# Performance work log

Measured on AMD Instinct MI355X. Metric: run time of the kernel, lower is better.

Reference implementation:

```python
import jax, jax.numpy as jnp
import numpy as np


def setup_inputs() -> dict:
    key = jax.random.key(0)
    k1, k2, k3 = jax.random.split(key, 3)
    B, H, HKV, S, D = 2, 32, 8, 2048, 128
    q = jax.random.normal(k1, (B, H, S, D), dtype=jnp.float32)
    k = jax.random.normal(k2, (B, HKV, S, D), dtype=jnp.float32)
    v = jax.random.normal(k3, (B, HKV, S, D), dtype=jnp.float32)
    return {"q": q, "k": k, "v": v}


def reference(q, k, v):
    # GQA: query head j attends with KV head j // num_groups (repeat_interleave
    # semantics). Instead of materializing repeated K/V, reshape Q into
    # [B, Hkv, G, S, D] and contract against shared KV heads directly.
    B, H, S, D = q.shape
    Hkv = k.shape[1]
    G = H // Hkv
    qg = q.reshape(B, Hkv, G, S, D)
    scale = 1.0 / jnp.sqrt(jnp.asarray(D, q.dtype))
    # scores: [B, Hkv, G, Sq, Sk]
    scores = jnp.einsum('bhgqd,bhkd->bhgqk', qg, k) * scale
    # is_causal=True: lower-triangular mask
    causal = jnp.tril(jnp.ones((S, S), dtype=bool))
    scores = jnp.where(causal, scores, jnp.finfo(scores.dtype).min)
    attn = jax.nn.softmax(scores, axis=-1)
    out = jnp.einsum('bhgqk,bhkd->bhgqd', attn, v)
    return out.reshape(B, H, S, D)
```

## Files before the change

### kernel.cpp

```cpp
#include <hip/hip_runtime.h>
#include <hip/hip_bf16.h>
#include <cstdint>

typedef __bf16 bf16;
typedef __bf16 bf16x8 __attribute__((ext_vector_type(8)));
typedef float f32x4 __attribute__((ext_vector_type(4)));
typedef __attribute__((address_space(3))) uint32_t lds_u32;
typedef const __attribute__((address_space(1))) uint32_t glb_u32;

#define B_ 2
#define H_ 32
#define HKV_ 8
#define S_ 2048
#define D_ 128
#define QT 128
#define KT 64
#define NQT (S_ / QT)
#define NTILES (S_ / KT)
#define TILE_ELEMS (KT * D_)
#define PST 72
#define NEG_BIG (-1.0e30f)
#define SCL 0.12751745f
#define DEFER_THR 8.0f

__device__ __forceinline__ bf16x8 cvt8p(float4 a, float4 b) {
  bf16x8 r = {(bf16)a.x, (bf16)a.y, (bf16)a.z, (bf16)a.w,
              (bf16)b.x, (bf16)b.y, (bf16)b.z, (bf16)b.w};
  return r;
}
__device__ __forceinline__ bf16x8 cvt8(const float* f) {
  return cvt8p(*(const float4*)f, *(const float4*)(f + 4));
}

__global__ __launch_bounds__(512) void prep(const float* __restrict__ k,
                                            const float* __restrict__ v,
                                            bf16* __restrict__ kws,
                                            bf16* __restrict__ vws) {
  __shared__ float Vf[KT * 129];
  const int blk = blockIdx.x;
  const int bhkv = blk >> 5, tile = blk & 31;
  const float* ks = k + ((size_t)bhkv * S_ + (size_t)tile * KT) * D_;
  const float* vs = v + ((size_t)bhkv * S_ + (size_t)tile * KT) * D_;
  bf16* kd = kws + (size_t)blk * TILE_ELEMS;
  bf16* vd = vws + (size_t)blk * TILE_ELEMS;
  const int t = threadIdx.x;
#pragma unroll
  for (int i = 0; i < 4; ++i) {
    int c = t + 512 * i, row = c >> 5, c4 = c & 31;
    *(float4*)&Vf[row * 129 + c4 * 4] = *(const float4*)(vs + row * D_ + c4 * 4);
  }
#pragma unroll
  for (int i = 0; i < 2; ++i) {
    int chunk = t + 512 * i, row = chunk >> 4, c16 = chunk & 15;
    int e = (c16 ^ (row & 7)) << 3;
    *(bf16x8*)&kd[chunk * 8] = cvt8(ks + row * D_ + e);
  }
  __syncthreads();
#pragma unroll
  for (int i = 0; i < 2; ++i) {
    int chunk = t + 512 * i, d = chunk >> 3, c8 = chunk & 7;
    int k0 = (c8 ^ (d & 7)) << 3;
    bf16x8 val;
#pragma unroll
    for (int kk = 0; kk < 8; ++kk) val[kk] = (bf16)Vf[(k0 + kk) * 129 + d];
    *(bf16x8*)&vd[chunk * 8] = val;
  }
}

__global__ __launch_bounds__(512, 4) void fa_mfma(
    const float* __restrict__ q, const bf16* __restrict__ kws,
    const bf16* __restrict__ vws, float* __restrict__ out) {
  __shared__ bf16 Kb2[2][TILE_ELEMS];
  __shared__ bf16 Vb[TILE_ELEMS];
  __shared__ bf16 Ps[8 * 16 * PST];

  const int tid = threadIdx.x, wave = tid >> 6, lane = tid & 63;
  const int col = lane & 15, quad = lane >> 4;
  const int bid = blockIdx.x;
  const int tqt = (NQT - 1) - (bid >> 6);
  const int bh = bid & 63, b = bh >> 5, h = bh & 31, hkv = h >> 2;
  const int bhkv = b * HKV_ + hkv;

  const float* qh = q + (size_t)(b * H_ + h) * S_ * D_;
  float* oh = out + (size_t)(b * H_ + h) * S_ * D_;
  const bf16* kg = kws + (size_t)(bhkv * NTILES) * TILE_ELEMS;
  const bf16* vg = vws + (size_t)(bhkv * NTILES) * TILE_ELEMS;
  const int q0 = tqt * QT;
  const int jmax = 2 * tqt + 1;

  bf16x8 qf[4];
  {
    const float* qrow = qh + (size_t)(q0 + wave * 16 + col) * D_ + quad * 8;
#pragma unroll
    for (int ks = 0; ks < 4; ++ks) qf[ks] = cvt8(qrow + ks * 32);
  }

  f32x4 o[8];
#pragma unroll
  for (int i = 0; i < 8; ++i) o[i] = (f32x4){0.f, 0.f, 0.f, 0.f};
  float m_i[4], lp[4];
#pragma unroll
  for (int r = 0; r < 4; ++r) { m_i[r] = NEG_BIG; lp[r] = 0.f; }

  const int qoff = (quad * 16) ^ ((col & 7) << 4);
  const int qx[4] = {qoff, qoff ^ 64, qoff ^ 128, qoff ^ 192};

  const int stoff = tid * 16;

  auto stageK = [&](int j, int buf) {
    const char* src = (const char*)(kg + (size_t)j * TILE_ELEMS) + stoff;
    char* dst = (char*)Kb2[buf] + stoff;
#pragma unroll
    for (int i = 0; i < 2; ++i)
      __builtin_amdgcn_global_load_lds((glb_u32*)(src + i * 8192),
                                       (lds_u32*)(dst + i * 8192), 16, 0, 0);
  };
  auto stageV = [&](int j) {
    const char* src = (const char*)(vg + (size_t)j * TILE_ELEMS) + stoff;
    char* dst = (char*)Vb + stoff;
#pragma unroll
    for (int i = 0; i < 2; ++i)
      __builtin_amdgcn_global_load_lds((glb_u32*)(src + i * 8192),
                                       (lds_u32*)(dst + i * 8192), 16, 0, 0);
  };

  stageK(0, 0);
  asm volatile("s_waitcnt vmcnt(0)" ::: "memory");
  __builtin_amdgcn_s_barrier();
  __builtin_amdgcn_sched_barrier(0);

  for (int j = 0; j <= jmax; ++j) {
    const int cur = j & 1;
    stageV(j);
    if (j < jmax) stageK(j + 1, cur ^ 1);

    const char* Kb = (const char*)Kb2[cur];

    float s[4][4];
    __builtin_amdgcn_s_setprio(1);
#pragma unroll
    for (int nt = 0; nt < 4; ++nt) {
      const char* An = Kb + (nt * 16 + col) * 256;
      f32x4 acc = (f32x4){0.f, 0.f, 0.f, 0.f};
#pragma unroll
      for (int ks = 0; ks < 4; ++ks) {
        bf16x8 kf = *(const bf16x8*)(An + qx[ks]);
        acc = __builtin_amdgcn_mfma_f32_16x16x32_bf16(qf[ks], kf, acc, 0, 0, 0);
      }
#pragma unroll
      for (int r = 0; r < 4; ++r) s[nt][r] = acc[r] * SCL;
    }
    __builtin_amdgcn_s_setprio(0);

    if (j >= 2 * tqt) {
      const int rel = j * KT - q0 - wave * 16;
#pragma unroll
      for (int nt = 0; nt < 4; ++nt) {
        int kc = rel + nt * 16 + col;
#pragma unroll
        for (int r = 0; r < 4; ++r)
          if (kc > quad * 4 + r) s[nt][r] = NEG_BIG;
      }
    }

    float mx[4];
#pragma unroll
    for (int r = 0; r < 4; ++r) {
      float m0 = fmaxf(fmaxf(s[0][r], s[1][r]), fmaxf(s[2][r], s[3][r]));
#pragma unroll
      for (int off = 1; off < 16; off <<= 1)
        m0 = fmaxf(m0, __shfl_xor(m0, off, 64));
      mx[r] = m0;
    }
    float need = fmaxf(fmaxf(mx[0] - m_i[0], mx[1] - m_i[1]),
                       fmaxf(mx[2] - m_i[2], mx[3] - m_i[3]));
    if (__any(need > DEFER_THR)) {
#pragma unroll
      for (int r = 0; r < 4; ++r) {
        float mnew = fmaxf(m_i[r], mx[r]);
        float alpha = exp2f(m_i[r] - mnew);
        lp[r] *= alpha;
        m_i[r] = mnew;
#pragma unroll
        for (int dt = 0; dt < 8; ++dt) o[dt][r] *= alpha;
      }
    }

    float p[4][4];
#pragma unroll
    for (int r = 0; r < 4; ++r) {
      float rs = 0.f;
#pragma unroll
      for (int nt = 0; nt < 4; ++nt) {
        float pv = exp2f(s[nt][r] - m_i[r]);
        p[nt][r] = pv;
        rs += pv;
      }
      lp[r] += rs;
    }

    bf16* pw = &Ps[wave * 16 * PST];
#pragma unroll
    for (int nt = 0; nt < 4; ++nt)
#pragma unroll
      for (int r = 0; r < 4; ++r)
        pw[(quad * 4 + r) * PST + nt * 16 + col] = (bf16)p[nt][r];

    if (j < jmax)
      asm volatile("s_waitcnt vmcnt(2) lgkmcnt(0)" ::: "memory");
    else
      asm volatile("s_waitcnt vmcnt(0) lgkmcnt(0)" ::: "memory");
    __builtin_amdgcn_s_barrier();
    __builtin_amdgcn_sched_barrier(0);

    bf16x8 pf[2];
#pragma unroll
    for (int ks = 0; ks < 2; ++ks)
      pf[ks] = *(const bf16x8*)&pw[col * PST + ks * 32 + quad * 8];

    __builtin_amdgcn_s_setprio(1);
#pragma unroll
    for (int dt = 0; dt < 8; ++dt) {
      const char* Av = (const char*)Vb + (dt * 16 + col) * 128;
#pragma unroll
      for (int ks = 0; ks < 2; ++ks) {
        bf16x8 vf = *(const bf16x8*)(Av + qx[ks]);
        o[dt] = __builtin_amdgcn_mfma_f32_16x16x32_bf16(pf[ks], vf, o[dt], 0, 0, 0);
      }
    }
    __builtin_amdgcn_s_setprio(0);

    if (j < jmax) {
      asm volatile("s_waitcnt vmcnt(0)" ::: "memory");
      __builtin_amdgcn_s_barrier();
      __builtin_amdgcn_sched_barrier(0);
    }
  }

#pragma unroll
  for (int r = 0; r < 4; ++r) {
    float l = lp[r];
#pragma unroll
    for (int off = 1; off < 16; off <<= 1)
      l += __shfl_xor(l, off, 64);
    float inv = 1.f / l;
    float* orow = oh + (size_t)(q0 + wave * 16 + quad * 4 + r) * D_;
#pragma unroll
    for (int dt = 0; dt < 8; ++dt)
      orow[dt * 16 + col] = o[dt][r] * inv;
  }
}

extern "C" void kernel_launch(void* const* d_in, const int* in_sizes, int n_in,
                              void* d_out, int out_size, void* d_ws, size_t ws_size,
                              hipStream_t stream) {
  const int QN = B_ * H_ * S_ * D_;
  int qi, ki, vi;
  if (in_sizes[0] == QN)      { qi = 0; ki = 1; vi = 2; }
  else if (in_sizes[1] == QN) { qi = 1; ki = 0; vi = 2; }
  else                        { qi = 2; ki = 0; vi = 1; }
  const float* q = (const float*)d_in[qi];
  const float* k = (const float*)d_in[ki];
  const float* v = (const float*)d_in[vi];
  float* out = (float*)d_out;

  bf16* kws = (bf16*)d_ws;
  bf16* vws = kws + (size_t)(B_ * HKV_) * NTILES * TILE_ELEMS;

  prep<<<dim3(B_ * HKV_ * NTILES), dim3(512), 0, stream>>>(k, v, kws, vws);
  fa_mfma<<<dim3(B_ * H_ * NQT), dim3(512), 0, stream>>>(q, kws, vws, out);
}
```

Before: 255.9 us.

## Transpose S/O MFMA layout and route P through registers via permlane swaps

Swaps the MFMA operand order so each lane holds one query row (column of S^T), which reduces the row max/sum reductions to two cross-lane shuffles and a single m_i/l per lane. The softmax probabilities are packed into bf16 pairs and redistributed into the PV A-operand layout using permlane32_swap and shfl_xor instead of a round trip through the LDS P buffer. This removes the P shared-memory buffer and its lgkmcnt wait, and makes the output stores float4-vectorized, at the cost of extra cross-lane permute instructions.

```diff
diff --git a/kernel.cpp b/kernel.cpp
--- a/kernel.cpp
+++ b/kernel.cpp
@@ -5,6 +5,7 @@
 typedef __bf16 bf16;
 typedef __bf16 bf16x8 __attribute__((ext_vector_type(8)));
 typedef float f32x4 __attribute__((ext_vector_type(4)));
+typedef unsigned int u32;
 typedef __attribute__((address_space(3))) uint32_t lds_u32;
 typedef const __attribute__((address_space(1))) uint32_t glb_u32;
 
@@ -18,7 +19,6 @@
 #define NQT (S_ / QT)
 #define NTILES (S_ / KT)
 #define TILE_ELEMS (KT * D_)
-#define PST 72
 #define NEG_BIG (-1.0e30f)
 #define SCL 0.12751745f
 #define DEFER_THR 8.0f
@@ -30,6 +30,11 @@
 }
 __device__ __forceinline__ bf16x8 cvt8(const float* f) {
   return cvt8p(*(const float4*)f, *(const float4*)(f + 4));
+}
+__device__ __forceinline__ u32 pk2(float lo, float hi) {
+  union { bf16 h[2]; u32 w; } u;
+  u.h[0] = (bf16)lo; u.h[1] = (bf16)hi;
+  return u.w;
 }
 
 __global__ __launch_bounds__(512) void prep(const float* __restrict__ k,
@@ -72,7 +77,6 @@
     const bf16* __restrict__ vws, float* __restrict__ out) {
   __shared__ bf16 Kb2[2][TILE_ELEMS];
   __shared__ bf16 Vb[TILE_ELEMS];
-  __shared__ bf16 Ps[8 * 16 * PST];
 
   const int tid = threadIdx.x, wave = tid >> 6, lane = tid & 63;
   const int col = lane & 15, quad = lane >> 4;
@@ -98,9 +102,7 @@
   f32x4 o[8];
 #pragma unroll
   for (int i = 0; i < 8; ++i) o[i] = (f32x4){0.f, 0.f, 0.f, 0.f};
-  float m_i[4], lp[4];
-#pragma unroll
-  for (int r = 0; r < 4; ++r) { m_i[r] = NEG_BIG; lp[r] = 0.f; }
+  float m_i = NEG_BIG, lp = 0.f;
 
   const int qoff = (quad * 16) ^ ((col & 7) << 4);
   const int qx[4] = {qoff, qoff ^ 64, qoff ^ 128, qoff ^ 192};
@@ -145,7 +147,7 @@
 #pragma unroll
       for (int ks = 0; ks < 4; ++ks) {
         bf16x8 kf = *(const bf16x8*)(An + qx[ks]);
-        acc = __builtin_amdgcn_mfma_f32_16x16x32_bf16(qf[ks], kf, acc, 0, 0, 0);
+        acc = __builtin_amdgcn_mfma_f32_16x16x32_bf16(kf, qf[ks], acc, 0, 0, 0);
       }
 #pragma unroll
       for (int r = 0; r < 4; ++r) s[nt][r] = acc[r] * SCL;
@@ -155,69 +157,68 @@
     if (j >= 2 * tqt) {
       const int rel = j * KT - q0 - wave * 16;
 #pragma unroll
-      for (int nt = 0; nt < 4; ++nt) {
-        int kc = rel + nt * 16 + col;
+      for (int nt = 0; nt < 4; ++nt)
 #pragma unroll
         for (int r = 0; r < 4; ++r)
-          if (kc > quad * 4 + r) s[nt][r] = NEG_BIG;
-      }
-    }
-
-    float mx[4];
-#pragma unroll
-    for (int r = 0; r < 4; ++r) {
-      float m0 = fmaxf(fmaxf(s[0][r], s[1][r]), fmaxf(s[2][r], s[3][r]));
-#pragma unroll
-      for (int off = 1; off < 16; off <<= 1)
-        m0 = fmaxf(m0, __shfl_xor(m0, off, 64));
-      mx[r] = m0;
-    }
-    float need = fmaxf(fmaxf(mx[0] - m_i[0], mx[1] - m_i[1]),
-                       fmaxf(mx[2] - m_i[2], mx[3] - m_i[3]));
-    if (__any(need > DEFER_THR)) {
+          if (rel + nt * 16 + quad * 4 + r > col) s[nt][r] = NEG_BIG;
+    }
+
+    float mx = s[0][0];
+#pragma unroll
+    for (int nt = 0; nt < 4; ++nt)
+#pragma unroll
+      for (int r = 0; r < 4; ++r) mx = fmaxf(mx, s[nt][r]);
+    mx = fmaxf(mx, __shfl_xor(mx, 16, 64));
+    mx = fmaxf(mx, __shfl_xor(mx, 32, 64));
+
+    if (__any(mx - m_i > DEFER_THR)) {
+      float mnew = fmaxf(m_i, mx);
+      float alpha = exp2f(m_i - mnew);
+      lp *= alpha;
+      m_i = mnew;
+#pragma unroll
+      for (int dt = 0; dt < 8; ++dt) o[dt] *= alpha;
+    }
+
+    float rs = 0.f;
+#pragma unroll
+    for (int nt = 0; nt < 4; ++nt)
 #pragma unroll
       for (int r = 0; r < 4; ++r) {
-        float mnew = fmaxf(m_i[r], mx[r]);
-        float alpha = exp2f(m_i[r] - mnew);
-        lp[r] *= alpha;
-        m_i[r] = mnew;
-#pragma unroll
-        for (int dt = 0; dt < 8; ++dt) o[dt][r] *= alpha;
-      }
-    }
-
-    float p[4][4];
-#pragma unroll
-    for (int r = 0; r < 4; ++r) {
-      float rs = 0.f;
-#pragma unroll
-      for (int nt = 0; nt < 4; ++nt) {
-        float pv = exp2f(s[nt][r] - m_i[r]);
-        p[nt][r] = pv;
-        rs += pv;
-      }
-      lp[r] += rs;
-    }
-
-    bf16* pw = &Ps[wave * 16 * PST];
-#pragma unroll
-    for (int nt = 0; nt < 4; ++nt)
-#pragma unroll
-      for (int r = 0; r < 4; ++r)
-        pw[(quad * 4 + r) * PST + nt * 16 + col] = (bf16)p[nt][r];
+        s[nt][r] = exp2f(s[nt][r] - m_i);
+        rs += s[nt][r];
+      }
+    lp += rs;
+
+    u32 pk_[4][2];
+#pragma unroll
+    for (int nt = 0; nt < 4; ++nt) {
+      pk_[nt][0] = pk2(s[nt][0], s[nt][1]);
+      pk_[nt][1] = pk2(s[nt][2], s[nt][3]);
+    }
+    const bool oddq = (quad & 1);
+    union W8 { u32 w[4]; bf16x8 h; } pf[2];
+#pragma unroll
+    for (int ks = 0; ks < 2; ++ks)
+#pragma unroll
+      for (int p = 0; p < 2; ++p) {
+        auto sw = __builtin_amdgcn_permlane32_swap(pk_[2 * ks][p],
+                                                   pk_[2 * ks + 1][p],
+                                                   false, false);
+        u32 Qp = (u32)sw[0], Rp = (u32)sw[1];
+        u32 Tp = (u32)__shfl_xor((int)Qp, 16, 64);
+        u32 Sp = (u32)__shfl_xor((int)Rp, 16, 64);
+        pf[ks].w[p] = oddq ? Sp : Qp;
+        pf[ks].w[2 + p] = oddq ? Rp : Tp;
+      }
 
     if (j < jmax)
-      asm volatile("s_waitcnt vmcnt(2) lgkmcnt(0)" ::: "memory");
+      asm volatile("s_waitcnt vmcnt(2)" ::: "memory");
     else
-      asm volatile("s_waitcnt vmcnt(0) lgkmcnt(0)" ::: "memory");
+      asm volatile("s_waitcnt vmcnt(0)" ::: "memory");
     __builtin_amdgcn_s_barrier();
     __builtin_amdgcn_sched_barrier(0);
 
-    bf16x8 pf[2];
-#pragma unroll
-    for (int ks = 0; ks < 2; ++ks)
-      pf[ks] = *(const bf16x8*)&pw[col * PST + ks * 32 + quad * 8];
-
     __builtin_amdgcn_s_setprio(1);
 #pragma unroll
     for (int dt = 0; dt < 8; ++dt) {
@@ -225,7 +226,7 @@
 #pragma unroll
       for (int ks = 0; ks < 2; ++ks) {
         bf16x8 vf = *(const bf16x8*)(Av + qx[ks]);
-        o[dt] = __builtin_amdgcn_mfma_f32_16x16x32_bf16(pf[ks], vf, o[dt], 0, 0, 0);
+        o[dt] = __builtin_amdgcn_mfma_f32_16x16x32_bf16(vf, pf[ks].h, o[dt], 0, 0, 0);
       }
     }
     __builtin_amdgcn_s_setprio(0);
@@ -237,17 +238,15 @@
     }
   }
 
-#pragma unroll
-  for (int r = 0; r < 4; ++r) {
-    float l = lp[r];
-#pragma unroll
-    for (int off = 1; off < 16; off <<= 1)
-      l += __shfl_xor(l, off, 64);
-    float inv = 1.f / l;
-    float* orow = oh + (size_t)(q0 + wave * 16 + quad * 4 + r) * D_;
-#pragma unroll
-    for (int dt = 0; dt < 8; ++dt)
-      orow[dt * 16 + col] = o[dt][r] * inv;
+  float l = lp;
+  l += __shfl_xor(l, 16, 64);
+  l += __shfl_xor(l, 32, 64);
+  const float inv = 1.f / l;
+  float* orow = oh + (size_t)(q0 + wave * 16 + col) * D_;
+#pragma unroll
+  for (int dt = 0; dt < 8; ++dt) {
+    f32x4 vout = o[dt] * inv;
+    *(f32x4*)&orow[dt * 16 + quad * 4] = vout;
   }
 }
 
```

New measurement: 241.1 us. 5.8% less time.
